# Kernel optimization log

Hardware: AMD Instinct MI355X
Metric: run time of the kernel (lower is better)

Reference implementation:

```python
import jax, jax.numpy as jnp
import numpy as np

D_MODEL = 2048
N_HEADS = 16
HEAD_DIM = 128
KV_RANK = 512


def setup_inputs() -> dict:
    key = jax.random.key(0)
    ks = jax.random.split(key, 6)
    s = lambda fan_in: 1.0 / np.sqrt(fan_in)
    return {
        "x": jax.random.normal(ks[0], (2, 2048, D_MODEL), dtype=jnp.float32),
        "Wq": jax.random.normal(ks[1], (D_MODEL, N_HEADS * HEAD_DIM), dtype=jnp.float32) * s(D_MODEL),
        "Wdown": jax.random.normal(ks[2], (D_MODEL, KV_RANK), dtype=jnp.float32) * s(D_MODEL),
        "Wk_up": jax.random.normal(ks[3], (KV_RANK, N_HEADS * HEAD_DIM), dtype=jnp.float32) * s(KV_RANK),
        "Wv_up": jax.random.normal(ks[4], (KV_RANK, N_HEADS * HEAD_DIM), dtype=jnp.float32) * s(KV_RANK),
        "Wo": jax.random.normal(ks[5], (N_HEADS * HEAD_DIM, D_MODEL), dtype=jnp.float32) * s(N_HEADS * HEAD_DIM),
    }


def reference(x, Wq, Wdown, Wk_up, Wv_up, Wo):
    B, T, _ = x.shape
    H, Dh = N_HEADS, HEAD_DIM
    # Q projection: (B,T,H,Dh) -> (B,H,T,Dh)
    Q = (x @ Wq).reshape(B, T, H, Dh).transpose(0, 2, 1, 3)
    # latent compression (this is the cached tensor)
    c = x @ Wdown  # (B, T, kv_lora_rank)
    # up-project latent to full K/V heads
    K = (c @ Wk_up).reshape(B, T, H, Dh).transpose(0, 2, 1, 3)
    V = (c @ Wv_up).reshape(B, T, H, Dh).transpose(0, 2, 1, 3)
    # causal SDPA (mask=None, past_kv=None -> is_causal=True), dropout=0
    scale = Dh ** (-0.5)
    scores = jnp.einsum("bhqd,bhkd->bhqk", Q, K) * scale
    causal = jnp.tril(jnp.ones((T, T), dtype=bool))
    scores = jnp.where(causal[None, None], scores, jnp.finfo(scores.dtype).min)
    attn = jax.nn.softmax(scores, axis=-1)
    out = jnp.einsum("bhqk,bhkd->bhqd", attn, V)
    out = out.transpose(0, 2, 1, 3).reshape(B, T, H * Dh)
    return out @ Wo, c
```

## Files before the change

### kernel.cpp

```cpp
#include <hip/hip_runtime.h>

typedef short bf16x8 __attribute__((ext_vector_type(8)));
typedef float f32x4 __attribute__((ext_vector_type(4)));

__device__ __forceinline__ void async16(const void* g, const void* l) {
  __builtin_amdgcn_global_load_lds(
      (const __attribute__((address_space(1))) unsigned int*)g,
      (__attribute__((address_space(3))) unsigned int*)(void*)(uintptr_t)l,
      16, 0, 0);
}

__device__ __forceinline__ unsigned short f2b(float f) {
  unsigned int u = __float_as_uint(f);
  u += 0x7fffu + ((u >> 16) & 1u);
  return (unsigned short)(u >> 16);
}

__global__ __launch_bounds__(256) void cast_f32_bf16(
    const float* __restrict__ in, unsigned short* __restrict__ out, int n) {
  int i = (blockIdx.x * 256 + threadIdx.x) * 4;
  if (i < n) {
    float4 v = *(const float4*)(in + i);
    ushort4 o;
    o.x = f2b(v.x); o.y = f2b(v.y); o.z = f2b(v.z); o.w = f2b(v.w);
    *(ushort4*)(out + i) = o;
  }
}

__global__ __launch_bounds__(256) void transpose_cast(
    const float* __restrict__ in, unsigned short* __restrict__ out,
    int K, int N) {
  __shared__ __align__(16) unsigned short tile[64][65];
  const int k0 = blockIdx.y * 64, n0 = blockIdx.x * 64;
  const int tid = threadIdx.x;
  const int r = tid >> 4, c4 = tid & 15;
#pragma unroll
  for (int p = 0; p < 4; ++p) {
    int row = p * 16 + r;
    float4 v = *(const float4*)(in + (size_t)(k0 + row) * N + n0 + c4 * 4);
    tile[c4 * 4 + 0][row] = f2b(v.x);
    tile[c4 * 4 + 1][row] = f2b(v.y);
    tile[c4 * 4 + 2][row] = f2b(v.z);
    tile[c4 * 4 + 3][row] = f2b(v.w);
  }
  __syncthreads();
#pragma unroll
  for (int p = 0; p < 4; ++p) {
    int nr = p * 16 + r;
    ushort4 o;
    o.x = tile[nr][c4 * 4 + 0];
    o.y = tile[nr][c4 * 4 + 1];
    o.z = tile[nr][c4 * 4 + 2];
    o.w = tile[nr][c4 * 4 + 3];
    *(ushort4*)(out + (size_t)(n0 + nr) * K + k0 + c4 * 4) = o;
  }
}

__global__ __launch_bounds__(256) void transpose_bf16(
    const unsigned short* __restrict__ in, unsigned short* __restrict__ out,
    int K, int N) {
  __shared__ __align__(16) unsigned short tile[64][65];
  const int k0 = blockIdx.y * 64, n0 = blockIdx.x * 64;
  const int tid = threadIdx.x;
  const int r = tid >> 4, c4 = tid & 15;
#pragma unroll
  for (int p = 0; p < 4; ++p) {
    int row = p * 16 + r;
    ushort4 v = *(const ushort4*)(in + (size_t)(k0 + row) * N + n0 + c4 * 4);
    tile[c4 * 4 + 0][row] = v.x;
    tile[c4 * 4 + 1][row] = v.y;
    tile[c4 * 4 + 2][row] = v.z;
    tile[c4 * 4 + 3][row] = v.w;
  }
  __syncthreads();
#pragma unroll
  for (int p = 0; p < 4; ++p) {
    int nr = p * 16 + r;
    ushort4 o;
    o.x = tile[nr][c4 * 4 + 0];
    o.y = tile[nr][c4 * 4 + 1];
    o.z = tile[nr][c4 * 4 + 2];
    o.w = tile[nr][c4 * 4 + 3];
    *(ushort4*)(out + (size_t)(n0 + nr) * K + k0 + c4 * 4) = o;
  }
}

__global__ __launch_bounds__(256) void gemm_bt(
    const unsigned short* __restrict__ A, const unsigned short* __restrict__ BT,
    unsigned short* __restrict__ Cb, float* __restrict__ Cf, int M, int N, int K) {
  __shared__ __align__(16) unsigned short sA[128 * 64];
  __shared__ __align__(16) unsigned short sB[128 * 64];
  const int tid = threadIdx.x;
  const int wave = tid >> 6, lane = tid & 63;
  const int quad = lane >> 4, cl = lane & 15;
  const int m0 = blockIdx.y * 128, n0 = blockIdx.x * 128;
  const int wm = (wave >> 1) * 64, wn = (wave & 1) * 64;
  (void)M;

  f32x4 acc[4][4] = {};

  const unsigned short* gA = A + (size_t)(m0 + wave * 32 + (lane >> 3)) * K + (lane & 7) * 8;
  const unsigned short* gB = BT + (size_t)(n0 + wave * 32 + (lane >> 3)) * K + (lane & 7) * 8;
  char* lA = (char*)sA + (wave * 32) * 128;
  char* lB = (char*)sB + (wave * 32) * 128;

  for (int kt = 0; kt < K; kt += 64) {
#pragma unroll
    for (int r = 0; r < 4; ++r) {
      async16(gA + (size_t)r * 8 * K + kt, lA + r * 8 * 128);
      async16(gB + (size_t)r * 8 * K + kt, lB + r * 8 * 128);
    }
    __syncthreads();
#pragma unroll
    for (int kk = 0; kk < 64; kk += 32) {
      bf16x8 af[4], bfr[4];
#pragma unroll
      for (int i = 0; i < 4; ++i)
        af[i] = *(const bf16x8*)((const char*)sA + (wm + i * 16 + cl) * 128 + kk * 2 + quad * 16);
#pragma unroll
      for (int j = 0; j < 4; ++j)
        bfr[j] = *(const bf16x8*)((const char*)sB + (wn + j * 16 + cl) * 128 + kk * 2 + quad * 16);
#pragma unroll
      for (int i = 0; i < 4; ++i)
#pragma unroll
        for (int j = 0; j < 4; ++j)
          acc[i][j] = __builtin_amdgcn_mfma_f32_16x16x32_bf16(af[i], bfr[j], acc[i][j], 0, 0, 0);
    }
    __syncthreads();
  }
#pragma unroll
  for (int i = 0; i < 4; ++i)
#pragma unroll
    for (int j = 0; j < 4; ++j)
#pragma unroll
      for (int r = 0; r < 4; ++r) {
        int row = m0 + wm + i * 16 + quad * 4 + r;
        int col = n0 + wn + j * 16 + cl;
        float v = acc[i][j][r];
        if (Cb) Cb[(size_t)row * N + col] = f2b(v);
        if (Cf) Cf[(size_t)row * N + col] = v;
      }
}

__global__ __launch_bounds__(256) void mla_attn(
    const unsigned short* __restrict__ Qm, const unsigned short* __restrict__ Km,
    const unsigned short* __restrict__ Vt, unsigned short* __restrict__ Om, int T) {
  const int ld = 2048;
  const int ldv = 4096;
  __shared__ __align__(16) unsigned short sK[64 * 128];
  __shared__ __align__(16) unsigned short sVT[128 * 64];
  __shared__ __align__(16) unsigned short sP[64 * 64];
  const int h = blockIdx.y, b = blockIdx.z;
  const int tid = threadIdx.x, wave = tid >> 6, lane = tid & 63;
  const int quad = lane >> 4, cl = lane & 15;
  const int nq = T / 64;
  const float scale2 = 0.08838834764831845f * 1.4426950408889634f;

  for (int phase = 0; phase < 2; ++phase) {
    const int qt = phase ? (nq - 1 - blockIdx.x) : blockIdx.x;

    bf16x8 qf[4];
    {
      const unsigned short* Qg =
          Qm + (size_t)(b * T + qt * 64 + wave * 16 + cl) * ld + h * 128 + quad * 8;
#pragma unroll
      for (int kk = 0; kk < 4; ++kk)
        qf[kk] = *(const bf16x8*)(Qg + kk * 32);
    }

    float m_i[4], l_i[4];
    f32x4 acc_o[8] = {};
#pragma unroll
    for (int r = 0; r < 4; ++r) { m_i[r] = -1e30f; l_i[r] = 0.f; }

    for (int kt = 0; kt <= qt; ++kt) {
      const unsigned short* Kg = Km + (size_t)(b * T + kt * 64) * ld + h * 128;
      const unsigned short* Vg = Vt + (size_t)(h * 128) * ldv + (size_t)b * T + kt * 64;
      __syncthreads();
#pragma unroll
      for (int r = 0; r < 4; ++r) {
        int c0 = r * 256 + wave * 64;
        int c = c0 + lane;
        int row = c >> 4, j = (c & 15) ^ (row & 7);
        async16(Kg + (size_t)row * ld + j * 8, (char*)sK + c0 * 16);
        int d = c >> 3, jv = (c & 7) ^ (d & 7);
        async16(Vg + (size_t)d * ldv + jv * 8, (char*)sVT + c0 * 16);
      }
      __syncthreads();

      f32x4 s[4] = {};
#pragma unroll
      for (int kk = 0; kk < 4; ++kk) {
#pragma unroll
        for (int j = 0; j < 4; ++j) {
          int t = j * 16 + cl;
          int jp = (kk * 4 + quad) ^ (t & 7);
          bf16x8 bk = *(const bf16x8*)((const char*)sK + (t * 16 + jp) * 16);
          s[j] = __builtin_amdgcn_mfma_f32_16x16x32_bf16(qf[kk], bk, s[j], 0, 0, 0);
        }
      }

      const bool need_mask = (kt == qt);
#pragma unroll
      for (int r = 0; r < 4; ++r) {
        int q_l = wave * 16 + quad * 4 + r;
        float mx = -1e30f;
#pragma unroll
        for (int j = 0; j < 4; ++j) {
          float v = s[j][r] * scale2;
          if (need_mask) {
            int t_l = j * 16 + cl;
            if (t_l > q_l) v = -1e30f;
          }
          s[j][r] = v;
          mx = fmaxf(mx, v);
        }
#pragma unroll
        for (int off = 1; off < 16; off <<= 1)
          mx = fmaxf(mx, __shfl_xor(mx, off));
        float m_new = fmaxf(m_i[r], mx);
        float alpha = exp2f(m_i[r] - m_new);
        m_i[r] = m_new;
        float rs = 0.f;
#pragma unroll
        for (int j = 0; j < 4; ++j) {
          float p = exp2f(s[j][r] - m_new);
          s[j][r] = p;
          rs += p;
        }
#pragma unroll
        for (int off = 1; off < 16; off <<= 1)
          rs += __shfl_xor(rs, off);
        l_i[r] = l_i[r] * alpha + rs;
#pragma unroll
        for (int jd = 0; jd < 8; ++jd)
          acc_o[jd][r] *= alpha;
      }

#pragma unroll
      for (int j = 0; j < 4; ++j)
#pragma unroll
        for (int r = 0; r < 4; ++r) {
          int q = wave * 16 + quad * 4 + r;
          int swz = (q & 7) ^ (((q >> 3) & 1) << 1);
          int t = j * 16 + cl;
          int jp = (t >> 3) ^ swz;
          sP[(q * 8 + jp) * 8 + (t & 7)] = f2b(s[j][r]);
        }

#pragma unroll
      for (int kk2 = 0; kk2 < 2; ++kk2) {
        int q = wave * 16 + cl;
        int swz = (q & 7) ^ (((q >> 3) & 1) << 1);
        int jp = (kk2 * 4 + quad) ^ swz;
        bf16x8 ap = *(const bf16x8*)((const char*)sP + (q * 8 + jp) * 16);
#pragma unroll
        for (int jd = 0; jd < 8; ++jd) {
          int d = jd * 16 + cl;
          int jpv = (kk2 * 4 + quad) ^ (d & 7);
          bf16x8 bv = *(const bf16x8*)((const char*)sVT + (d * 8 + jpv) * 16);
          acc_o[jd] = __builtin_amdgcn_mfma_f32_16x16x32_bf16(ap, bv, acc_o[jd], 0, 0, 0);
        }
      }
    }

#pragma unroll
    for (int r = 0; r < 4; ++r) {
      float inv = 1.f / l_i[r];
      int row = b * T + qt * 64 + wave * 16 + quad * 4 + r;
#pragma unroll
      for (int jd = 0; jd < 8; ++jd)
        Om[(size_t)row * ld + h * 128 + jd * 16 + cl] = f2b(acc_o[jd][r] * inv);
    }
  }
}

extern "C" void kernel_launch(void* const* d_in, const int* in_sizes, int n_in,
                              void* d_out, int out_size, void* d_ws, size_t ws_size,
                              hipStream_t stream) {
  (void)in_sizes; (void)n_in; (void)out_size; (void)ws_size;
  const int B = 2, T = 2048, Dm = 2048, H = 16, Dh = 128, R = 512;
  const int M = B * T;
  const float* x     = (const float*)d_in[0];
  const float* Wq    = (const float*)d_in[1];
  const float* Wdown = (const float*)d_in[2];
  const float* Wkup  = (const float*)d_in[3];
  const float* Wvup  = (const float*)d_in[4];
  const float* Wo    = (const float*)d_in[5];

  float* out  = (float*)d_out;
  float* cout = out + (size_t)M * Dm;

  unsigned short* ws  = (unsigned short*)d_ws;
  unsigned short* WqT = ws;
  unsigned short* WoT = WqT + (size_t)Dm * Dm;
  unsigned short* WdT = WoT + (size_t)Dm * Dm;
  unsigned short* WkT = WdT + (size_t)R * Dm;
  unsigned short* WvT = WkT + (size_t)Dm * R;
  unsigned short* xb  = WvT + (size_t)Dm * R;
  unsigned short* cb  = xb + (size_t)M * Dm;
  unsigned short* Qb  = cb + (size_t)M * R;
  unsigned short* Kb  = Qb + (size_t)M * Dm;
  unsigned short* Vb  = Kb + (size_t)M * Dm;
  unsigned short* Vtb = Vb + (size_t)M * Dm;
  unsigned short* AO  = xb;

  cast_f32_bf16<<<(M * Dm) / 1024, 256, 0, stream>>>(x, xb, M * Dm);
  transpose_cast<<<dim3(32, 32), 256, 0, stream>>>(Wq, WqT, Dm, Dm);
  transpose_cast<<<dim3(32, 32), 256, 0, stream>>>(Wo, WoT, Dm, Dm);
  transpose_cast<<<dim3(8, 32), 256, 0, stream>>>(Wdown, WdT, Dm, R);
  transpose_cast<<<dim3(32, 8), 256, 0, stream>>>(Wkup, WkT, R, Dm);
  transpose_cast<<<dim3(32, 8), 256, 0, stream>>>(Wvup, WvT, R, Dm);

  gemm_bt<<<dim3(R / 128, M / 128), 256, 0, stream>>>(xb, WdT, cb, cout, M, R, Dm);
  gemm_bt<<<dim3(Dm / 128, M / 128), 256, 0, stream>>>(xb, WqT, Qb, nullptr, M, Dm, Dm);
  gemm_bt<<<dim3(Dm / 128, M / 128), 256, 0, stream>>>(cb, WkT, Kb, nullptr, M, Dm, R);
  gemm_bt<<<dim3(Dm / 128, M / 128), 256, 0, stream>>>(cb, WvT, Vb, nullptr, M, Dm, R);

  transpose_bf16<<<dim3(Dm / 64, M / 64), 256, 0, stream>>>(Vb, Vtb, M, Dm);

  mla_attn<<<dim3(T / 128, H, B), 256, 0, stream>>>(Qb, Kb, Vtb, AO, T);

  gemm_bt<<<dim3(Dm / 128, M / 128), 256, 0, stream>>>(AO, WoT, nullptr, out, M, Dm, Dm);
  (void)Dh; (void)H;
}
```

Measured before the change: 428.0 us.

## Run paired causal query tiles concurrently in 512-thread attention blocks sharing K/V loads

The attention kernel now runs the light and heavy query tiles of each pair at the same time in two 4-wave groups of a 512-thread block, rather than one after the other. Each K/V tile loaded into LDS is reused by both groups. The softmax scale is folded into the Q projection GEMM epilogue, and the row sums are computed by an MFMA against a ones vector instead of shuffle reductions. P is converted to bf16 by truncation instead of rounding. This cuts serial phases, per-element multiplies and cross-lane shuffles, but the light group sits idle for many iterations, and truncation adds a small precision bias.

```diff
diff --git a/kernel.cpp b/kernel.cpp
--- a/kernel.cpp
+++ b/kernel.cpp
@@ -14,6 +14,9 @@
   unsigned int u = __float_as_uint(f);
   u += 0x7fffu + ((u >> 16) & 1u);
   return (unsigned short)(u >> 16);
+}
+__device__ __forceinline__ unsigned short f2b_trunc(float f) {
+  return (unsigned short)(__float_as_uint(f) >> 16);
 }
 
 __global__ __launch_bounds__(256) void cast_f32_bf16(
@@ -87,7 +90,8 @@
 
 __global__ __launch_bounds__(256) void gemm_bt(
     const unsigned short* __restrict__ A, const unsigned short* __restrict__ BT,
-    unsigned short* __restrict__ Cb, float* __restrict__ Cf, int M, int N, int K) {
+    unsigned short* __restrict__ Cb, float* __restrict__ Cf, int M, int N, int K,
+    float alpha) {
   __shared__ __align__(16) unsigned short sA[128 * 64];
   __shared__ __align__(16) unsigned short sB[128 * 64];
   const int tid = threadIdx.x;
@@ -136,124 +140,123 @@
       for (int r = 0; r < 4; ++r) {
         int row = m0 + wm + i * 16 + quad * 4 + r;
         int col = n0 + wn + j * 16 + cl;
-        float v = acc[i][j][r];
+        float v = acc[i][j][r] * alpha;
         if (Cb) Cb[(size_t)row * N + col] = f2b(v);
         if (Cf) Cf[(size_t)row * N + col] = v;
       }
 }
 
-__global__ __launch_bounds__(256) void mla_attn(
+__global__ __launch_bounds__(512) void mla_attn(
     const unsigned short* __restrict__ Qm, const unsigned short* __restrict__ Km,
     const unsigned short* __restrict__ Vt, unsigned short* __restrict__ Om, int T) {
   const int ld = 2048;
   const int ldv = 4096;
   __shared__ __align__(16) unsigned short sK[64 * 128];
   __shared__ __align__(16) unsigned short sVT[128 * 64];
-  __shared__ __align__(16) unsigned short sP[64 * 64];
-  const int h = blockIdx.y, b = blockIdx.z;
+  __shared__ __align__(16) unsigned short sP[2][64 * 64];
+  const int h = blockIdx.x, j = blockIdx.y, b = blockIdx.z;
   const int tid = threadIdx.x, wave = tid >> 6, lane = tid & 63;
   const int quad = lane >> 4, cl = lane & 15;
-  const int nq = T / 64;
-  const float scale2 = 0.08838834764831845f * 1.4426950408889634f;
-
-  for (int phase = 0; phase < 2; ++phase) {
-    const int qt = phase ? (nq - 1 - blockIdx.x) : blockIdx.x;
-
-    bf16x8 qf[4];
-    {
-      const unsigned short* Qg =
-          Qm + (size_t)(b * T + qt * 64 + wave * 16 + cl) * ld + h * 128 + quad * 8;
-#pragma unroll
-      for (int kk = 0; kk < 4; ++kk)
-        qf[kk] = *(const bf16x8*)(Qg + kk * 32);
+  const int grp = wave >> 2, w4 = wave & 3;
+  const int qt = grp ? j : (31 - j);
+  const int qt_heavy = 31 - j;
+
+  bf16x8 qf[4];
+  {
+    const unsigned short* Qg =
+        Qm + (size_t)(b * T + qt * 64 + w4 * 16 + cl) * ld + h * 128 + quad * 8;
+#pragma unroll
+    for (int kk = 0; kk < 4; ++kk)
+      qf[kk] = *(const bf16x8*)(Qg + kk * 32);
+  }
+
+  bf16x8 vones;
+#pragma unroll
+  for (int z = 0; z < 8; ++z) vones[z] = (short)0x3f80;
+
+  float m_i[4], l_i[4];
+  f32x4 acc_o[8] = {};
+#pragma unroll
+  for (int r = 0; r < 4; ++r) { m_i[r] = -1e30f; l_i[r] = 0.f; }
+
+  for (int kt = 0; kt <= qt_heavy; ++kt) {
+    const unsigned short* Kg = Km + (size_t)(b * T + kt * 64) * ld + h * 128;
+    const unsigned short* Vg = Vt + (size_t)(h * 128) * ldv + (size_t)b * T + kt * 64;
+    __syncthreads();
+#pragma unroll
+    for (int r = 0; r < 2; ++r) {
+      int c0 = (r * 8 + wave) * 64;
+      int c = c0 + lane;
+      int row = c >> 4, jj = (c & 15) ^ (row & 7);
+      async16(Kg + (size_t)row * ld + jj * 8, (char*)sK + c0 * 16);
+      int d = c >> 3, jv = (c & 7) ^ (d & 7);
+      async16(Vg + (size_t)d * ldv + jv * 8, (char*)sVT + c0 * 16);
     }
-
-    float m_i[4], l_i[4];
-    f32x4 acc_o[8] = {};
-#pragma unroll
-    for (int r = 0; r < 4; ++r) { m_i[r] = -1e30f; l_i[r] = 0.f; }
-
-    for (int kt = 0; kt <= qt; ++kt) {
-      const unsigned short* Kg = Km + (size_t)(b * T + kt * 64) * ld + h * 128;
-      const unsigned short* Vg = Vt + (size_t)(h * 128) * ldv + (size_t)b * T + kt * 64;
-      __syncthreads();
-#pragma unroll
-      for (int r = 0; r < 4; ++r) {
-        int c0 = r * 256 + wave * 64;
-        int c = c0 + lane;
-        int row = c >> 4, j = (c & 15) ^ (row & 7);
-        async16(Kg + (size_t)row * ld + j * 8, (char*)sK + c0 * 16);
-        int d = c >> 3, jv = (c & 7) ^ (d & 7);
-        async16(Vg + (size_t)d * ldv + jv * 8, (char*)sVT + c0 * 16);
-      }
-      __syncthreads();
-
+    __syncthreads();
+
+    if (kt <= qt) {
       f32x4 s[4] = {};
 #pragma unroll
       for (int kk = 0; kk < 4; ++kk) {
 #pragma unroll
-        for (int j = 0; j < 4; ++j) {
-          int t = j * 16 + cl;
+        for (int jt = 0; jt < 4; ++jt) {
+          int t = jt * 16 + cl;
           int jp = (kk * 4 + quad) ^ (t & 7);
           bf16x8 bk = *(const bf16x8*)((const char*)sK + (t * 16 + jp) * 16);
-          s[j] = __builtin_amdgcn_mfma_f32_16x16x32_bf16(qf[kk], bk, s[j], 0, 0, 0);
+          s[jt] = __builtin_amdgcn_mfma_f32_16x16x32_bf16(qf[kk], bk, s[jt], 0, 0, 0);
         }
       }
 
       const bool need_mask = (kt == qt);
+      float alpha_r[4];
 #pragma unroll
       for (int r = 0; r < 4; ++r) {
-        int q_l = wave * 16 + quad * 4 + r;
+        int q_l = w4 * 16 + quad * 4 + r;
         float mx = -1e30f;
 #pragma unroll
-        for (int j = 0; j < 4; ++j) {
-          float v = s[j][r] * scale2;
+        for (int jt = 0; jt < 4; ++jt) {
+          float v = s[jt][r];
           if (need_mask) {
-            int t_l = j * 16 + cl;
+            int t_l = jt * 16 + cl;
             if (t_l > q_l) v = -1e30f;
           }
-          s[j][r] = v;
+          s[jt][r] = v;
           mx = fmaxf(mx, v);
         }
 #pragma unroll
         for (int off = 1; off < 16; off <<= 1)
           mx = fmaxf(mx, __shfl_xor(mx, off));
         float m_new = fmaxf(m_i[r], mx);
-        float alpha = exp2f(m_i[r] - m_new);
+        alpha_r[r] = exp2f(m_i[r] - m_new);
         m_i[r] = m_new;
-        float rs = 0.f;
-#pragma unroll
-        for (int j = 0; j < 4; ++j) {
-          float p = exp2f(s[j][r] - m_new);
-          s[j][r] = p;
-          rs += p;
+#pragma unroll
+        for (int jt = 0; jt < 4; ++jt)
+          s[jt][r] = exp2f(s[jt][r] - m_new);
+      }
+
+      f32x4 av = {alpha_r[0], alpha_r[1], alpha_r[2], alpha_r[3]};
+#pragma unroll
+      for (int jd = 0; jd < 8; ++jd) acc_o[jd] *= av;
+
+#pragma unroll
+      for (int jt = 0; jt < 4; ++jt)
+#pragma unroll
+        for (int r = 0; r < 4; ++r) {
+          int q = w4 * 16 + quad * 4 + r;
+          int swz = (q & 7) ^ (((q >> 3) & 1) << 1);
+          int t = jt * 16 + cl;
+          int jp = (t >> 3) ^ swz;
+          sP[grp][(q * 8 + jp) * 8 + (t & 7)] = f2b_trunc(s[jt][r]);
         }
-#pragma unroll
-        for (int off = 1; off < 16; off <<= 1)
-          rs += __shfl_xor(rs, off);
-        l_i[r] = l_i[r] * alpha + rs;
-#pragma unroll
-        for (int jd = 0; jd < 8; ++jd)
-          acc_o[jd][r] *= alpha;
-      }
-
-#pragma unroll
-      for (int j = 0; j < 4; ++j)
-#pragma unroll
-        for (int r = 0; r < 4; ++r) {
-          int q = wave * 16 + quad * 4 + r;
-          int swz = (q & 7) ^ (((q >> 3) & 1) << 1);
-          int t = j * 16 + cl;
-          int jp = (t >> 3) ^ swz;
-          sP[(q * 8 + jp) * 8 + (t & 7)] = f2b(s[j][r]);
-        }
-
+
+      f32x4 acc_l = {};
 #pragma unroll
       for (int kk2 = 0; kk2 < 2; ++kk2) {
-        int q = wave * 16 + cl;
+        int q = w4 * 16 + cl;
         int swz = (q & 7) ^ (((q >> 3) & 1) << 1);
         int jp = (kk2 * 4 + quad) ^ swz;
-        bf16x8 ap = *(const bf16x8*)((const char*)sP + (q * 8 + jp) * 16);
+        bf16x8 ap = *(const bf16x8*)((const char*)&sP[grp][0] + (q * 8 + jp) * 16);
+        acc_l = __builtin_amdgcn_mfma_f32_16x16x32_bf16(ap, vones, acc_l, 0, 0, 0);
 #pragma unroll
         for (int jd = 0; jd < 8; ++jd) {
           int d = jd * 16 + cl;
@@ -262,16 +265,19 @@
           acc_o[jd] = __builtin_amdgcn_mfma_f32_16x16x32_bf16(ap, bv, acc_o[jd], 0, 0, 0);
         }
       }
+#pragma unroll
+      for (int r = 0; r < 4; ++r)
+        l_i[r] = l_i[r] * alpha_r[r] + acc_l[r];
     }
-
-#pragma unroll
-    for (int r = 0; r < 4; ++r) {
-      float inv = 1.f / l_i[r];
-      int row = b * T + qt * 64 + wave * 16 + quad * 4 + r;
-#pragma unroll
-      for (int jd = 0; jd < 8; ++jd)
-        Om[(size_t)row * ld + h * 128 + jd * 16 + cl] = f2b(acc_o[jd][r] * inv);
-    }
+  }
+
+#pragma unroll
+  for (int r = 0; r < 4; ++r) {
+    float inv = 1.f / l_i[r];
+    int row = b * T + qt * 64 + w4 * 16 + quad * 4 + r;
+#pragma unroll
+    for (int jd = 0; jd < 8; ++jd)
+      Om[(size_t)row * ld + h * 128 + jd * 16 + cl] = f2b(acc_o[jd][r] * inv);
   }
 }
 
@@ -305,6 +311,8 @@
   unsigned short* Vtb = Vb + (size_t)M * Dm;
   unsigned short* AO  = xb;
 
+  const float scale2 = 0.08838834764831845f * 1.4426950408889634f;
+
   cast_f32_bf16<<<(M * Dm) / 1024, 256, 0, stream>>>(x, xb, M * Dm);
   transpose_cast<<<dim3(32, 32), 256, 0, stream>>>(Wq, WqT, Dm, Dm);
   transpose_cast<<<dim3(32, 32), 256, 0, stream>>>(Wo, WoT, Dm, Dm);
@@ -312,15 +320,15 @@
   transpose_cast<<<dim3(32, 8), 256, 0, stream>>>(Wkup, WkT, R, Dm);
   transpose_cast<<<dim3(32, 8), 256, 0, stream>>>(Wvup, WvT, R, Dm);
 
-  gemm_bt<<<dim3(R / 128, M / 128), 256, 0, stream>>>(xb, WdT, cb, cout, M, R, Dm);
-  gemm_bt<<<dim3(Dm / 128, M / 128), 256, 0, stream>>>(xb, WqT, Qb, nullptr, M, Dm, Dm);
-  gemm_bt<<<dim3(Dm / 128, M / 128), 256, 0, stream>>>(cb, WkT, Kb, nullptr, M, Dm, R);
-  gemm_bt<<<dim3(Dm / 128, M / 128), 256, 0, stream>>>(cb, WvT, Vb, nullptr, M, Dm, R);
+  gemm_bt<<<dim3(R / 128, M / 128), 256, 0, stream>>>(xb, WdT, cb, cout, M, R, Dm, 1.0f);
+  gemm_bt<<<dim3(Dm / 128, M / 128), 256, 0, stream>>>(xb, WqT, Qb, nullptr, M, Dm, Dm, scale2);
+  gemm_bt<<<dim3(Dm / 128, M / 128), 256, 0, stream>>>(cb, WkT, Kb, nullptr, M, Dm, R, 1.0f);
+  gemm_bt<<<dim3(Dm / 128, M / 128), 256, 0, stream>>>(cb, WvT, Vb, nullptr, M, Dm, R, 1.0f);
 
   transpose_bf16<<<dim3(Dm / 64, M / 64), 256, 0, stream>>>(Vb, Vtb, M, Dm);
 
-  mla_attn<<<dim3(T / 128, H, B), 256, 0, stream>>>(Qb, Kb, Vtb, AO, T);
-
-  gemm_bt<<<dim3(Dm / 128, M / 128), 256, 0, stream>>>(AO, WoT, nullptr, out, M, Dm, Dm);
+  mla_attn<<<dim3(H, T / 128, B), 512, 0, stream>>>(Qb, Kb, Vtb, AO, T);
+
+  gemm_bt<<<dim3(Dm / 128, M / 128), 256, 0, stream>>>(AO, WoT, nullptr, out, M, Dm, Dm, 1.0f);
   (void)Dh; (void)H;
 }
```

Result: slower. 439.7 us (+2.7%).
